# Performance work log

Measured on AMD Instinct MI355X. Metric: run time of the kernel, lower is better.

The kernel has to match this reference:

```python
import jax, jax.numpy as jnp
import numpy as np


def setup_inputs() -> dict:
    key = jax.random.key(0)
    k1, k2, k3, k4, k5 = jax.random.split(key, 5)
    B, S, IN, OUT, G = 8, 2048, 4096, 4096, 32
    NB = OUT * IN // G  # 524288 blocks
    x = jax.random.normal(k1, (B, S, IN), dtype=jnp.float32)
    # two int4 values packed per byte -> G//2 bytes per block
    weight_packed = jax.random.randint(k2, (NB, G // 2), 0, 256, dtype=jnp.int32)
    weight_scale = (jax.random.uniform(k3, (NB, 1)) * 0.02).astype(jnp.float16)
    weight_var_mask = jax.random.randint(k4, (NB,), 0, 2) > 0
    bias = jax.random.normal(k5, (OUT,), dtype=jnp.float32)
    return {"x": x, "weight_packed": weight_packed, "weight_scale": weight_scale,
            "weight_var_mask": weight_var_mask, "bias": bias}


def _block_dequantize_mixed(packed, scale, mask):
    # packed: [NB, G//2] int32 holding two uint4 per byte
    # scale:  [NB, 1] fp16 per-block scale; mask: [NB] bool (high-variance blocks keep full scale)
    q_lo = packed & 0xF
    q_hi = (packed >> 4) & 0xF
    q = jnp.stack([q_lo, q_hi], axis=-1).reshape(packed.shape[0], -1)  # [NB, G], interleaved
    scale_eff = scale.astype(jnp.float32) * jnp.where(mask[:, None], 1.0, 0.5)
    return (q.astype(jnp.float32) - 8.0) * scale_eff  # [NB, G]


def reference(x, weight_packed, weight_scale, weight_var_mask, bias):
    out_features = bias.shape[0]
    in_features = x.shape[-1]
    w = _block_dequantize_mixed(weight_packed, weight_scale, weight_var_mask)
    w = w.reshape(out_features, in_features)  # [OUT, IN]
    # y = x @ w^T + b
    return jnp.einsum('bsi,oi->bso', x, w) + bias
```

## Files before the change

### kernel.cpp

```cpp
#include <hip/hip_runtime.h>
#include <hip/hip_bf16.h>
#include <stdint.h>

#define M_TOT 16384
#define N_TOT 4096
#define K_TOT 4096
#define NB    524288

#define BM 256
#define BN 256
#define BK 64
#define NT (K_TOT / BK)

typedef __attribute__((ext_vector_type(8))) __bf16 bf16x8;
typedef __attribute__((ext_vector_type(4))) float f32x4;

#define BARF() do { asm volatile("" ::: "memory"); \
                    __builtin_amdgcn_s_barrier(); \
                    asm volatile("" ::: "memory"); } while (0)
#define VMW(n) asm volatile("s_waitcnt vmcnt(" #n ")" ::: "memory")

#define MFMA1(d, a, b) d = __builtin_amdgcn_mfma_f32_16x16x32_bf16(a, b, d, 0, 0, 0)
#define MFMA_PAIR(mb, A0, A1) do { \
  _Pragma("unroll") \
  for (int j_ = 0; j_ < 4; ++j_) { \
    MFMA1(acc[mb][j_],     A0[0], bF[j_][0]); \
    MFMA1(acc[mb][j_],     A0[1], bF[j_][1]); \
    MFMA1(acc[(mb)+1][j_], A1[0], bF[j_][0]); \
    MFMA1(acc[(mb)+1][j_], A1[1], bF[j_][1]); \
  } \
} while (0)

__global__ __launch_bounds__(256) void dequant_w(
    const int* __restrict__ packed,
    const float* __restrict__ scale,
    const int* __restrict__ mask,
    __hip_bfloat16* __restrict__ wout)
{
    int t = blockIdx.x * blockDim.x + threadIdx.x;
    const int4 pk = ((const int4*)packed)[t];
    int nb = t >> 2;
    float se = scale[nb] * (mask[nb] ? 1.0f : 0.5f);
    int vals[4] = { pk.x, pk.y, pk.z, pk.w };
    __hip_bfloat16 o[8];
#pragma unroll
    for (int j = 0; j < 4; ++j) {
        int v = vals[j];
        o[2*j]   = __float2bfloat16((float)((v & 0xF) - 8) * se);
        o[2*j+1] = __float2bfloat16((float)(((v >> 4) & 0xF) - 8) * se);
    }
    int4 st;
    __builtin_memcpy(&st, o, 16);
    ((int4*)wout)[t] = st;
}

__global__ __launch_bounds__(256) void cvt_x(
    const float* __restrict__ x, __hip_bfloat16* __restrict__ xb)
{
    int t = blockIdx.x * blockDim.x + threadIdx.x;
    const float4* xp = (const float4*)x;
    float4 a = xp[2*t], b = xp[2*t + 1];
    __hip_bfloat16 o[8] = {
        __float2bfloat16(a.x), __float2bfloat16(a.y),
        __float2bfloat16(a.z), __float2bfloat16(a.w),
        __float2bfloat16(b.x), __float2bfloat16(b.y),
        __float2bfloat16(b.z), __float2bfloat16(b.w)
    };
    int4 st;
    __builtin_memcpy(&st, o, 16);
    ((int4*)xb)[t] = st;
}

__global__ __launch_bounds__(512, 2) void gemm_bt(
    const __hip_bfloat16* __restrict__ A,
    const __hip_bfloat16* __restrict__ Bw,
    const float* __restrict__ bias,
    float* __restrict__ C)
{
    __shared__ __align__(16) char lds[131072];

    const int tid  = threadIdx.x;
    const int lane = tid & 63;
    const int wave = tid >> 6;
    const int wm = wave >> 2;
    const int wn = wave & 3;

    const int wg = (blockIdx.x & 7) * 128 + (blockIdx.x >> 3);
    const int mt = wg & 63;
    const int nt = wg >> 6;
    const int m0 = mt * BM;
    const int n0 = nt * BN;

    const int srow = tid >> 3;
    const int scb  = ((tid & 7) * 16) ^ (((tid >> 3) & 7) << 4);
    const char* gA = (const char*)A  + ((size_t)(m0 + srow) * K_TOT) * 2 + scb;
    const char* gB = (const char*)Bw + ((size_t)(n0 + srow) * K_TOT) * 2 + scb;
    char* lA = (char*)lds + tid * 16;
    char* lB = (char*)lds + 32768 + tid * 16;

    auto stA4 = [&](int t) {
        if (t >= NT) t -= 2;
        const int p = t & 1;
        const size_t kb = (size_t)t * (BK * 2);
#pragma unroll
        for (int r = 0; r < 4; ++r) {
            __builtin_amdgcn_global_load_lds(
                (const __attribute__((address_space(1))) void*)
                    (gA + kb + (size_t)r * 64 * K_TOT * 2),
                (__attribute__((address_space(3))) void*)
                    (lA + p * 65536 + r * 8192), 16, 0, 0);
        }
    };
    auto stB2 = [&](int t, int h) {
        if (t >= NT) t -= 2;
        const int p = t & 1;
        const size_t kb = (size_t)t * (BK * 2);
#pragma unroll
        for (int s = 0; s < 2; ++s) {
            const int r = 2 * h + s;
            __builtin_amdgcn_global_load_lds(
                (const __attribute__((address_space(1))) void*)
                    (gB + kb + (size_t)r * 64 * K_TOT * 2),
                (__attribute__((address_space(3))) void*)
                    (lB + p * 65536 + r * 8192), 16, 0, 0);
        }
    };

    const int swz  = (lane & 7) << 4;
    const int pcb0 = (((lane >> 4) * 16) + 0)  ^ swz;
    const int pcb1 = (((lane >> 4) * 16) + 64) ^ swz;
    int arow[8], brow[4];
#pragma unroll
    for (int i = 0; i < 8; ++i) arow[i] = (wm * 128 + i * 16 + (lane & 15)) * 128;
#pragma unroll
    for (int j = 0; j < 4; ++j) brow[j] = (wn * 64 + j * 16 + (lane & 15)) * 128;

    f32x4 acc[8][4] = {};

    const char* ldsA0 = (const char*)lds;
    const char* ldsB0 = (const char*)lds + 32768;
    const char* ldsA1 = (const char*)lds + 65536;
    const char* ldsB1 = (const char*)lds + 98304;

#define TILE_BLOCK(Ap, Bp, STG_A, STG_B0, STG_B1) do { \
    bf16x8 bF[4][2], aCur[2][2], aNxt[2][2]; \
     \
    _Pragma("unroll") \
    for (int j_ = 0; j_ < 4; ++j_) { \
        bF[j_][0] = *(const bf16x8*)((Bp) + brow[j_] + pcb0); \
        bF[j_][1] = *(const bf16x8*)((Bp) + brow[j_] + pcb1); \
    } \
    _Pragma("unroll") \
    for (int m_ = 0; m_ < 2; ++m_) { \
        aCur[m_][0] = *(const bf16x8*)((Ap) + arow[m_] + pcb0); \
        aCur[m_][1] = *(const bf16x8*)((Ap) + arow[m_] + pcb1); \
        aNxt[m_][0] = *(const bf16x8*)((Ap) + arow[2 + m_] + pcb0); \
        aNxt[m_][1] = *(const bf16x8*)((Ap) + arow[2 + m_] + pcb1); \
    } \
    STG_A; \
    __builtin_amdgcn_s_setprio(1); MFMA_PAIR(0, aCur[0], aCur[1]); \
    __builtin_amdgcn_s_setprio(0); \
    BARF(); \
     \
    _Pragma("unroll") \
    for (int m_ = 0; m_ < 2; ++m_) { \
        aCur[m_][0] = *(const bf16x8*)((Ap) + arow[4 + m_] + pcb0); \
        aCur[m_][1] = *(const bf16x8*)((Ap) + arow[4 + m_] + pcb1); \
    } \
    STG_B0; \
    __builtin_amdgcn_s_setprio(1); MFMA_PAIR(2, aNxt[0], aNxt[1]); \
    __builtin_amdgcn_s_setprio(0); \
    BARF(); \
     \
    _Pragma("unroll") \
    for (int m_ = 0; m_ < 2; ++m_) { \
        aNxt[m_][0] = *(const bf16x8*)((Ap) + arow[6 + m_] + pcb0); \
        aNxt[m_][1] = *(const bf16x8*)((Ap) + arow[6 + m_] + pcb1); \
    } \
    STG_B1; \
    __builtin_amdgcn_s_setprio(1); MFMA_PAIR(4, aCur[0], aCur[1]); \
    __builtin_amdgcn_s_setprio(0); \
    BARF(); \
     \
    __builtin_amdgcn_s_setprio(1); MFMA_PAIR(6, aNxt[0], aNxt[1]); \
    __builtin_amdgcn_s_setprio(0); \
    VMW(4); \
    BARF(); \
} while (0)

    stB2(0, 0); stB2(0, 1); stA4(0); stB2(1, 0); stB2(1, 1);
    VMW(4);
    BARF();

    for (int it = 0; it < NT / 2; ++it) {
        const int ta = 2 * it, tb = ta + 1;
        TILE_BLOCK(ldsA0, ldsB0, stA4(tb),     stB2(ta + 2, 0), stB2(ta + 2, 1));
        TILE_BLOCK(ldsA1, ldsB1, stA4(ta + 2), stB2(tb + 2, 0), stB2(tb + 2, 1));
    }
#undef TILE_BLOCK

    const int cl = lane & 15;
    const int rq = (lane >> 4) * 4;
#pragma unroll
    for (int j = 0; j < 4; ++j) {
        const int col = n0 + wn * 64 + j * 16 + cl;
        const float bv = bias[col];
#pragma unroll
        for (int i = 0; i < 8; ++i) {
            const size_t rbase = (size_t)(m0 + wm * 128 + i * 16 + rq);
#pragma unroll
            for (int r = 0; r < 4; ++r) {
                C[(rbase + r) * N_TOT + col] = acc[i][j][r] + bv;
            }
        }
    }
    VMW(0);
}

extern "C" void kernel_launch(void* const* d_in, const int* in_sizes, int n_in,
                              void* d_out, int out_size, void* d_ws, size_t ws_size,
                              hipStream_t stream) {
    const float* x      = (const float*)d_in[0];
    const int*   wp     = (const int*)d_in[1];
    const float* wscale = (const float*)d_in[2];
    const int*   wmask  = (const int*)d_in[3];
    const float* bias   = (const float*)d_in[4];
    float*       out    = (float*)d_out;

    __hip_bfloat16* Wb = (__hip_bfloat16*)d_ws;
    __hip_bfloat16* Xb = (__hip_bfloat16*)((char*)d_ws + (size_t)N_TOT * K_TOT * 2);

    dequant_w<<<(NB * 4) / 256, 256, 0, stream>>>(wp, wscale, wmask, Wb);
    cvt_x<<<((size_t)M_TOT * K_TOT / 8) / 256, 256, 0, stream>>>(x, Xb);
    gemm_bt<<<(M_TOT / BM) * (N_TOT / BN), 512, 0, stream>>>(Xb, Wb, bias, out);
}
```

Measured before the change: 897.0 us.

## Merge dequant and x-convert into one grid-stride kernel; reorder MFMA by k-half

The separate weight-dequantize and x-to-bf16 kernels become a single persistent grid-stride launch, with 1024 blocks on the weights and 3072 on the activations. This removes one launch and lets the two memory-bound passes run at the same time. Inside the GEMM tile, the LDS fragment loads are split by k-half, and the MFMAs are reordered to issue all k=0 products before the k=1 products. This is meant to let the first MFMAs start before the second-half fragments arrive. The reordering may change register pressure and the dependency chains on each accumulator.

```diff
diff --git a/kernel.cpp b/kernel.cpp
--- a/kernel.cpp
+++ b/kernel.cpp
@@ -21,54 +21,60 @@
 #define VMW(n) asm volatile("s_waitcnt vmcnt(" #n ")" ::: "memory")
 
 #define MFMA1(d, a, b) d = __builtin_amdgcn_mfma_f32_16x16x32_bf16(a, b, d, 0, 0, 0)
-#define MFMA_PAIR(mb, A0, A1) do { \
+#define HALF(mb, A0k, A1k, Bk, ks) do { \
   _Pragma("unroll") \
   for (int j_ = 0; j_ < 4; ++j_) { \
-    MFMA1(acc[mb][j_],     A0[0], bF[j_][0]); \
-    MFMA1(acc[mb][j_],     A0[1], bF[j_][1]); \
-    MFMA1(acc[(mb)+1][j_], A1[0], bF[j_][0]); \
-    MFMA1(acc[(mb)+1][j_], A1[1], bF[j_][1]); \
+    MFMA1(acc[mb][j_],     A0k, Bk[j_][ks]); \
+    MFMA1(acc[(mb)+1][j_], A1k, Bk[j_][ks]); \
   } \
 } while (0)
 
-__global__ __launch_bounds__(256) void dequant_w(
+#define DQ_BLOCKS 1024
+#define CV_BLOCKS 3072
+__global__ __launch_bounds__(256) void prep(
     const int* __restrict__ packed,
     const float* __restrict__ scale,
     const int* __restrict__ mask,
-    __hip_bfloat16* __restrict__ wout)
+    __hip_bfloat16* __restrict__ wout,
+    const float* __restrict__ x,
+    __hip_bfloat16* __restrict__ xb)
 {
-    int t = blockIdx.x * blockDim.x + threadIdx.x;
-    const int4 pk = ((const int4*)packed)[t];
-    int nb = t >> 2;
-    float se = scale[nb] * (mask[nb] ? 1.0f : 0.5f);
-    int vals[4] = { pk.x, pk.y, pk.z, pk.w };
-    __hip_bfloat16 o[8];
-#pragma unroll
-    for (int j = 0; j < 4; ++j) {
-        int v = vals[j];
-        o[2*j]   = __float2bfloat16((float)((v & 0xF) - 8) * se);
-        o[2*j+1] = __float2bfloat16((float)(((v >> 4) & 0xF) - 8) * se);
+    if (blockIdx.x < DQ_BLOCKS) {
+        const size_t total = (size_t)NB * 4;
+        for (size_t t = (size_t)blockIdx.x * blockDim.x + threadIdx.x;
+             t < total; t += (size_t)DQ_BLOCKS * 256) {
+            const int4 pk = ((const int4*)packed)[t];
+            size_t nb = t >> 2;
+            float se = scale[nb] * (mask[nb] ? 1.0f : 0.5f);
+            int vals[4] = { pk.x, pk.y, pk.z, pk.w };
+            __hip_bfloat16 o[8];
+#pragma unroll
+            for (int j = 0; j < 4; ++j) {
+                int v = vals[j];
+                o[2*j]   = __float2bfloat16((float)((v & 0xF) - 8) * se);
+                o[2*j+1] = __float2bfloat16((float)(((v >> 4) & 0xF) - 8) * se);
+            }
+            int4 st;
+            __builtin_memcpy(&st, o, 16);
+            ((int4*)wout)[t] = st;
+        }
+    } else {
+        const size_t total = (size_t)M_TOT * K_TOT / 8;
+        const float4* xp = (const float4*)x;
+        for (size_t t = (size_t)(blockIdx.x - DQ_BLOCKS) * blockDim.x + threadIdx.x;
+             t < total; t += (size_t)CV_BLOCKS * 256) {
+            float4 a = xp[2*t], b = xp[2*t + 1];
+            __hip_bfloat16 o[8] = {
+                __float2bfloat16(a.x), __float2bfloat16(a.y),
+                __float2bfloat16(a.z), __float2bfloat16(a.w),
+                __float2bfloat16(b.x), __float2bfloat16(b.y),
+                __float2bfloat16(b.z), __float2bfloat16(b.w)
+            };
+            int4 st;
+            __builtin_memcpy(&st, o, 16);
+            ((int4*)xb)[t] = st;
+        }
     }
-    int4 st;
-    __builtin_memcpy(&st, o, 16);
-    ((int4*)wout)[t] = st;
-}
-
-__global__ __launch_bounds__(256) void cvt_x(
-    const float* __restrict__ x, __hip_bfloat16* __restrict__ xb)
-{
-    int t = blockIdx.x * blockDim.x + threadIdx.x;
-    const float4* xp = (const float4*)x;
-    float4 a = xp[2*t], b = xp[2*t + 1];
-    __hip_bfloat16 o[8] = {
-        __float2bfloat16(a.x), __float2bfloat16(a.y),
-        __float2bfloat16(a.z), __float2bfloat16(a.w),
-        __float2bfloat16(b.x), __float2bfloat16(b.y),
-        __float2bfloat16(b.z), __float2bfloat16(b.w)
-    };
-    int4 st;
-    __builtin_memcpy(&st, o, 16);
-    ((int4*)xb)[t] = st;
 }
 
 __global__ __launch_bounds__(512, 2) void gemm_bt(
@@ -146,43 +152,57 @@
     bf16x8 bF[4][2], aCur[2][2], aNxt[2][2]; \
      \
     _Pragma("unroll") \
-    for (int j_ = 0; j_ < 4; ++j_) { \
+    for (int j_ = 0; j_ < 4; ++j_) \
         bF[j_][0] = *(const bf16x8*)((Bp) + brow[j_] + pcb0); \
-        bF[j_][1] = *(const bf16x8*)((Bp) + brow[j_] + pcb1); \
-    } \
     _Pragma("unroll") \
     for (int m_ = 0; m_ < 2; ++m_) { \
         aCur[m_][0] = *(const bf16x8*)((Ap) + arow[m_] + pcb0); \
+        aNxt[m_][0] = *(const bf16x8*)((Ap) + arow[2 + m_] + pcb0); \
+    } \
+    _Pragma("unroll") \
+    for (int j_ = 0; j_ < 4; ++j_) \
+        bF[j_][1] = *(const bf16x8*)((Bp) + brow[j_] + pcb1); \
+    _Pragma("unroll") \
+    for (int m_ = 0; m_ < 2; ++m_) { \
         aCur[m_][1] = *(const bf16x8*)((Ap) + arow[m_] + pcb1); \
-        aNxt[m_][0] = *(const bf16x8*)((Ap) + arow[2 + m_] + pcb0); \
         aNxt[m_][1] = *(const bf16x8*)((Ap) + arow[2 + m_] + pcb1); \
     } \
     STG_A; \
-    __builtin_amdgcn_s_setprio(1); MFMA_PAIR(0, aCur[0], aCur[1]); \
-    __builtin_amdgcn_s_setprio(0); \
-    BARF(); \
-     \
-    _Pragma("unroll") \
-    for (int m_ = 0; m_ < 2; ++m_) { \
+    __builtin_amdgcn_s_setprio(1); \
+    HALF(0, aCur[0][0], aCur[1][0], bF, 0); \
+    HALF(0, aCur[0][1], aCur[1][1], bF, 1); \
+    __builtin_amdgcn_s_setprio(0); \
+    BARF(); \
+     \
+    _Pragma("unroll") \
+    for (int m_ = 0; m_ < 2; ++m_) \
         aCur[m_][0] = *(const bf16x8*)((Ap) + arow[4 + m_] + pcb0); \
+    _Pragma("unroll") \
+    for (int m_ = 0; m_ < 2; ++m_) \
         aCur[m_][1] = *(const bf16x8*)((Ap) + arow[4 + m_] + pcb1); \
-    } \
     STG_B0; \
-    __builtin_amdgcn_s_setprio(1); MFMA_PAIR(2, aNxt[0], aNxt[1]); \
-    __builtin_amdgcn_s_setprio(0); \
-    BARF(); \
-     \
-    _Pragma("unroll") \
-    for (int m_ = 0; m_ < 2; ++m_) { \
+    __builtin_amdgcn_s_setprio(1); \
+    HALF(2, aNxt[0][0], aNxt[1][0], bF, 0); \
+    HALF(2, aNxt[0][1], aNxt[1][1], bF, 1); \
+    __builtin_amdgcn_s_setprio(0); \
+    BARF(); \
+     \
+    _Pragma("unroll") \
+    for (int m_ = 0; m_ < 2; ++m_) \
         aNxt[m_][0] = *(const bf16x8*)((Ap) + arow[6 + m_] + pcb0); \
+    _Pragma("unroll") \
+    for (int m_ = 0; m_ < 2; ++m_) \
         aNxt[m_][1] = *(const bf16x8*)((Ap) + arow[6 + m_] + pcb1); \
-    } \
     STG_B1; \
-    __builtin_amdgcn_s_setprio(1); MFMA_PAIR(4, aCur[0], aCur[1]); \
-    __builtin_amdgcn_s_setprio(0); \
-    BARF(); \
-     \
-    __builtin_amdgcn_s_setprio(1); MFMA_PAIR(6, aNxt[0], aNxt[1]); \
+    __builtin_amdgcn_s_setprio(1); \
+    HALF(4, aCur[0][0], aCur[1][0], bF, 0); \
+    HALF(4, aCur[0][1], aCur[1][1], bF, 1); \
+    __builtin_amdgcn_s_setprio(0); \
+    BARF(); \
+     \
+    __builtin_amdgcn_s_setprio(1); \
+    HALF(6, aNxt[0][0], aNxt[1][0], bF, 0); \
+    HALF(6, aNxt[0][1], aNxt[1][1], bF, 1); \
     __builtin_amdgcn_s_setprio(0); \
     VMW(4); \
     BARF(); \
@@ -230,7 +250,6 @@
     __hip_bfloat16* Wb = (__hip_bfloat16*)d_ws;
     __hip_bfloat16* Xb = (__hip_bfloat16*)((char*)d_ws + (size_t)N_TOT * K_TOT * 2);
 
-    dequant_w<<<(NB * 4) / 256, 256, 0, stream>>>(wp, wscale, wmask, Wb);
-    cvt_x<<<((size_t)M_TOT * K_TOT / 8) / 256, 256, 0, stream>>>(x, Xb);
+    prep<<<DQ_BLOCKS + CV_BLOCKS, 256, 0, stream>>>(wp, wscale, wmask, Wb, x, Xb);
     gemm_bt<<<(M_TOT / BM) * (N_TOT / BN), 512, 0, stream>>>(Xb, Wb, bias, out);
 }
```

New measurement: 906.7 us. No clear change (+1.1%).
